# Kernel tuning notes

Hardware: AMD Instinct MI355X
Metric: run time of the kernel (lower is better)

Reference implementation:

```python
import jax, jax.numpy as jnp
import numpy as np
import math

B, T, C = 8, 1024, 512
H = 8
HD = C // H  # 64
MAX_REL = 64 + 4  # args.block_size + args.time_cond


def setup_inputs() -> dict:
    key = jax.random.key(0)
    ks = jax.random.split(key, 12)
    xavier = lambda k, shape: jax.random.uniform(
        k, shape, jnp.float32, -1.0, 1.0) * math.sqrt(6.0 / (shape[0] + shape[1]))
    return {
        "x": jax.random.normal(ks[0], (B, T, C), jnp.float32),
        "Wq": xavier(ks[1], (C, C)), "bq": jnp.zeros((C,), jnp.float32),
        "Wk": xavier(ks[2], (C, C)), "bk": jnp.zeros((C,), jnp.float32),
        "Wv": xavier(ks[3], (C, C)), "bv": jnp.zeros((C,), jnp.float32),
        "Wo": xavier(ks[4], (C, C)), "bo": jnp.zeros((C,), jnp.float32),
        "rel_k": xavier(ks[5], (2 * MAX_REL + 1, HD)),
        "rel_v": xavier(ks[6], (2 * MAX_REL + 1, HD)),
    }


def _rel_index(t):
    # clipped relative distance matrix, shifted to [0, 2*MAX_REL]
    r = jnp.arange(t)
    dist = jnp.clip(r[None, :] - r[:, None], -MAX_REL, MAX_REL)
    return dist + MAX_REL  # (T, T) int32


def reference(x, Wq, bq, Wk, bk, Wv, bv, Wo, bo, rel_k, rel_v):
    b, t, c = x.shape
    h, hd = H, HD
    q = x @ Wq + bq
    k = x @ Wk + bk
    v = x @ Wv + bv
    rq = q.reshape(b, t, h, hd).transpose(0, 2, 1, 3)  # (B,H,T,hd)
    rk = k.reshape(b, t, h, hd).transpose(0, 2, 1, 3)
    rv = v.reshape(b, t, h, hd).transpose(0, 2, 1, 3)

    idx = _rel_index(t)                 # (T,T)
    rk2 = rel_k[idx]                    # (T,T,hd)
    rv2 = rel_v[idx]                    # (T,T,hd)

    attn1 = jnp.einsum("bhqd,bhkd->bhqk", rq, rk)
    attn2 = jnp.einsum("bhqd,qkd->bhqk", rq, rk2)
    # NOTE: original scales by 1/sqrt(embed_dim) (k.size(-1) == C), not head_dim
    attn = jax.nn.softmax((attn1 + attn2) * (1.0 / math.sqrt(c)), axis=-1)

    w1 = jnp.einsum("bhqk,bhkd->bhqd", attn, rv)
    w2 = jnp.einsum("bhqk,qkd->bhqd", attn, rv2)
    out = (w1 + w2).transpose(0, 2, 1, 3).reshape(b, t, c)
    return out @ Wo + bo
```

## Files before the change

### kernel.cpp

```cpp
#include <hip/hip_runtime.h>
#include <stdint.h>

#define Bb 8
#define Tt 1024
#define Cc 512
#define Hh 8
#define HD 64
#define MREL 68
#define NR 137
#define NRP 160
#define A2S 168
#define SCALE 0.044194173824159216f
#define KSCL  0.063763016845703125f

typedef unsigned short u16;
typedef unsigned int u32;
using u16x4  = __attribute__((ext_vector_type(4))) u16;
using u16x8  = __attribute__((ext_vector_type(8))) u16;
using f32x4  = __attribute__((ext_vector_type(4))) float;
using bf16x8 = __attribute__((ext_vector_type(8))) __bf16;

__device__ __forceinline__ u16 f2bf(float f) {
  u32 u = __builtin_bit_cast(u32, f);
  u += 0x7FFF + ((u >> 16) & 1);
  return (u16)(u >> 16);
}
__device__ __forceinline__ float bf2f(u16 v) {
  return __builtin_bit_cast(float, (u32)v << 16);
}
__device__ __forceinline__ bf16x8 as_bf8(u16x8 v) { return __builtin_bit_cast(bf16x8, v); }
__device__ __forceinline__ float fexp2(float x) {
  float r; asm("v_exp_f32 %0, %1" : "=v"(r) : "v"(x)); return r;
}

#define MFMA16(a, b, c) __builtin_amdgcn_mfma_f32_16x16x32_bf16((a), (b), (c), 0, 0, 0)
#define PSWZ(row, col) ((col) ^ (((row) & 7) << 3))

__global__ __launch_bounds__(256) void relv_prep(
    const float* __restrict__ rel_v, u16* __restrict__ rvT)
{
  int i = blockIdx.x * 256 + threadIdx.x;
  if (i < HD * NRP) {
    int d = i / NRP, r = i - d * NRP;
    rvT[i] = (r < NR) ? f2bf(rel_v[r * HD + d]) : (u16)0;
  }
}

__global__ __launch_bounds__(256) void w_prep(
    const float* __restrict__ Wq, const float* __restrict__ Wk,
    const float* __restrict__ Wv, const float* __restrict__ Wo,
    u16* __restrict__ WqT, u16* __restrict__ WkT,
    u16* __restrict__ WvT, u16* __restrict__ WoT)
{
  const float* W = blockIdx.y == 0 ? Wq : blockIdx.y == 1 ? Wk
                  : blockIdx.y == 2 ? Wv : Wo;
  u16* WT = blockIdx.y == 0 ? WqT : blockIdx.y == 1 ? WkT
           : blockIdx.y == 2 ? WvT : WoT;
  int i = blockIdx.x * 256 + threadIdx.x;
  int n = i >> 7, k4 = (i & 127) * 4;
  u16x4 o;
  #pragma unroll
  for (int j = 0; j < 4; ++j) o[j] = f2bf(W[(size_t)(k4 + j) * Cc + n]);
  *(u16x4*)&WT[(size_t)n * Cc + k4] = o;
}

__global__ __launch_bounds__(256) void qkv_gemm(
    const float* __restrict__ x,
    const u16* __restrict__ WqT, const u16* __restrict__ WkT,
    const u16* __restrict__ WvT,
    const float* __restrict__ bq, const float* __restrict__ bk,
    const float* __restrict__ bv,
    u16* __restrict__ Qb, u16* __restrict__ Kb, u16* __restrict__ VTb)
{
  __shared__ u16 Xs[64][40];
  __shared__ u16 WTs[3][64][40];

  const u16* Wp[3] = {WqT, WkT, WvT};
  const float* bp[3] = {bq, bk, bv};

  const int tid = threadIdx.x;
  const int wv_ = tid >> 6;
  const int l   = tid & 63;
  const int lr  = l & 15, lg = l >> 4;
  const int m0  = blockIdx.x * 64;
  const int n0  = blockIdx.y * 64;
  const int srow = tid >> 2, scol = (tid & 3) * 8;

  f32x4 acc[3][4];
  #pragma unroll
  for (int a = 0; a < 3; ++a)
    #pragma unroll
    for (int b = 0; b < 4; ++b) acc[a][b] = (f32x4){0.f, 0.f, 0.f, 0.f};

  for (int k0 = 0; k0 < Cc; k0 += 32) {
    {
      const float* xp = x + (size_t)(m0 + srow) * Cc + k0 + scol;
      f32x4 v0 = *(const f32x4*)xp;
      f32x4 v1 = *(const f32x4*)(xp + 4);
      u16x8 o = {f2bf(v0[0]), f2bf(v0[1]), f2bf(v0[2]), f2bf(v0[3]),
                 f2bf(v1[0]), f2bf(v1[1]), f2bf(v1[2]), f2bf(v1[3])};
      *(u16x8*)&Xs[srow][scol] = o;
    }
    #pragma unroll
    for (int q3 = 0; q3 < 3; ++q3) {
      u16x8 w = *(const u16x8*)(Wp[q3] + (size_t)(n0 + srow) * Cc + k0 + scol);
      *(u16x8*)&WTs[q3][srow][scol] = w;
    }
    __syncthreads();

    bf16x8 a = as_bf8(*(const u16x8*)&Xs[wv_ * 16 + lr][lg * 8]);
    #pragma unroll
    for (int q3 = 0; q3 < 3; ++q3) {
      #pragma unroll
      for (int nt = 0; nt < 4; ++nt) {
        bf16x8 b = as_bf8(*(const u16x8*)&WTs[q3][nt * 16 + lr][lg * 8]);
        acc[q3][nt] = MFMA16(a, b, acc[q3][nt]);
      }
    }
    __syncthreads();
  }

  const int bidx = m0 >> 10;
  #pragma unroll
  for (int q3 = 0; q3 < 3; ++q3) {
    #pragma unroll
    for (int nt = 0; nt < 4; ++nt) {
      int n = n0 + nt * 16 + lr;
      int h = n >> 6, d = n & 63;
      float bias = bp[q3][n];
      #pragma unroll
      for (int i = 0; i < 4; ++i) {
        int m = m0 + wv_ * 16 + lg * 4 + i;
        int t = m & (Tt - 1);
        u16 o = f2bf(acc[q3][nt][i] + bias);
        size_t bh = (size_t)(bidx * Hh + h);
        if (q3 == 0)      Qb[(bh * Tt + t) * HD + d] = o;
        else if (q3 == 1) Kb[(bh * Tt + t) * HD + d] = o;
        else              VTb[(bh * HD + d) * Tt + t] = o;
      }
    }
  }
}

__global__ __launch_bounds__(256, 4) void attn_kernel(
    const u16* __restrict__ Qb, const u16* __restrict__ Kb,
    const u16* __restrict__ VTb, const u16* __restrict__ rvT,
    const float* __restrict__ rel_k,
    u16* __restrict__ AO)
{
  __shared__ u16 P[16][1024];
  __shared__ u16 S2a2[16][A2S];
  __shared__ float red[2][4][16];
  __shared__ float rowrcp[16];

  const int tid = threadIdx.x;
  const int wv_ = tid >> 6, l = tid & 63;
  const int lr = l & 15, lg = l >> 4;
  const int bh = blockIdx.x;
  const int q0 = blockIdx.y * 16;
  const int bidx = bh >> 3, h = bh & 7;

  const u16* Qh = Qb  + (size_t)bh * Tt * HD;
  const u16* Kh = Kb  + (size_t)bh * Tt * HD;
  const u16* Vh = VTb + (size_t)bh * HD * Tt;

  bf16x8 aQ0 = as_bf8(*(const u16x8*)(Qh + (size_t)(q0 + lr) * HD + lg * 8));
  bf16x8 aQ1 = as_bf8(*(const u16x8*)(Qh + (size_t)(q0 + lr) * HD + 32 + lg * 8));

  const u16* kbase = Kh + (size_t)(wv_ * 16 + lr) * HD + lg * 8;
  u16x8 c0 = *(const u16x8*)(kbase);
  u16x8 c1 = *(const u16x8*)(kbase + 32);

  for (int ct = wv_; ct < 9; ct += 4) {
    int r = ct * 16 + lr;
    f32x4 acc = {0.f, 0.f, 0.f, 0.f};
    #pragma unroll
    for (int d0 = 0; d0 < 64; d0 += 32) {
      u16x8 bbits = {0, 0, 0, 0, 0, 0, 0, 0};
      if (r < NR) {
        f32x4 v0 = *(const f32x4*)(rel_k + (size_t)r * HD + d0 + lg * 8);
        f32x4 v1 = *(const f32x4*)(rel_k + (size_t)r * HD + d0 + lg * 8 + 4);
        bbits = (u16x8){f2bf(v0[0]), f2bf(v0[1]), f2bf(v0[2]), f2bf(v0[3]),
                        f2bf(v1[0]), f2bf(v1[1]), f2bf(v1[2]), f2bf(v1[3])};
      }
      acc = MFMA16(d0 ? aQ1 : aQ0, as_bf8(bbits), acc);
    }
    #pragma unroll
    for (int i = 0; i < 4; ++i)
      S2a2[lg * 4 + i][ct * 16 + lr] = f2bf(acc[i] * KSCL);
  }
  __syncthreads();

  float ps[4]  = {0.f, 0.f, 0.f, 0.f};
  float ps0[4] = {0.f, 0.f, 0.f, 0.f};

  #pragma unroll
  for (int kt = 0; kt < 16; ++kt) {
    u16x8 n0{}, n1{};
    if (kt < 15) {
      n0 = *(const u16x8*)(kbase + (size_t)(kt + 1) * 64 * HD);
      n1 = *(const u16x8*)(kbase + (size_t)(kt + 1) * 64 * HD + 32);
    }
    int kc = kt * 64 + wv_ * 16 + lr;
    f32x4 acc = {0.f, 0.f, 0.f, 0.f};
    acc = MFMA16(aQ0, as_bf8(c0), acc);
    acc = MFMA16(aQ1, as_bf8(c1), acc);
    int b2 = kc - q0 - lg * 4;
    #pragma unroll
    for (int i = 0; i < 4; ++i) {
      int row = lg * 4 + i;
      int dr = b2 - i;
      dr = dr < -MREL ? -MREL : (dr > MREL ? MREL : dr);
      float p = fexp2(fmaf(acc[i], KSCL, bf2f(S2a2[row][dr + MREL])));
      ps[i] += p;
      if (kc <= q0 + row - MREL) ps0[i] += p;
      P[row][PSWZ(row, kc)] = f2bf(p);
    }
    if (kt < 15) { c0 = n0; c1 = n1; }
  }

  #pragma unroll
  for (int off = 1; off < 16; off <<= 1) {
    #pragma unroll
    for (int i = 0; i < 4; ++i) {
      ps[i]  += __shfl_xor(ps[i], off);
      ps0[i] += __shfl_xor(ps0[i], off);
    }
  }
  if (lr == 0) {
    #pragma unroll
    for (int i = 0; i < 4; ++i) {
      red[0][wv_][lg * 4 + i] = ps[i];
      red[1][wv_][lg * 4 + i] = ps0[i];
    }
  }

  const u16* vrow = Vh + (size_t)(wv_ * 16 + lr) * Tt + lg * 8;
  u16x8 vc0 = *(const u16x8*)(vrow);
  u16x8 vc1 = *(const u16x8*)(vrow + 32);

  __syncthreads();

  {
    int row = tid >> 4, c16 = tid & 15;
    int qg = q0 + row;
    float band = 0.f;
    for (int r = 1 + c16; r < NR - 1; r += 16) {
      int k = qg + r - MREL;
      u16 v = (k >= 0 && k < Tt) ? P[row][PSWZ(row, k)] : (u16)0;
      S2a2[row][r] = v;
      band += bf2f(v);
    }
    #pragma unroll
    for (int off = 1; off < 16; off <<= 1) band += __shfl_xor(band, off);
    for (int r = NR + c16; r < NRP; r += 16) S2a2[row][r] = 0;
    if (c16 == 0) {
      float t0 = red[0][0][row] + red[0][1][row] + red[0][2][row] + red[0][3][row];
      float t1 = red[1][0][row] + red[1][1][row] + red[1][2][row] + red[1][3][row];
      S2a2[row][0]      = f2bf(t1);
      S2a2[row][NR - 1] = f2bf(t0 - t1 - band);
      rowrcp[row] = 1.0f / t0;
    }
  }
  __syncthreads();

  f32x4 o0 = {0.f, 0.f, 0.f, 0.f}, o1 = {0.f, 0.f, 0.f, 0.f};
  #pragma unroll
  for (int kp = 0; kp < 15; ++kp) {
    u16x8 vn0 = *(const u16x8*)(vrow + kp * 64 + 64);
    u16x8 vn1 = *(const u16x8*)(vrow + kp * 64 + 96);
    bf16x8 a0 = as_bf8(*(const u16x8*)&P[lr][PSWZ(lr, kp * 64 + lg * 8)]);
    bf16x8 a1 = as_bf8(*(const u16x8*)&P[lr][PSWZ(lr, kp * 64 + 32 + lg * 8)]);
    o0 = MFMA16(a0, as_bf8(vc0), o0);
    o1 = MFMA16(a1, as_bf8(vc1), o1);
    vc0 = vn0; vc1 = vn1;
  }
  {
    bf16x8 a0 = as_bf8(*(const u16x8*)&P[lr][PSWZ(lr, 15 * 64 + lg * 8)]);
    bf16x8 a1 = as_bf8(*(const u16x8*)&P[lr][PSWZ(lr, 15 * 64 + 32 + lg * 8)]);
    o0 = MFMA16(a0, as_bf8(vc0), o0);
    o1 = MFMA16(a1, as_bf8(vc1), o1);
  }
  #pragma unroll
  for (int j = 0; j < 5; ++j) {
    u16x8 brv = *(const u16x8*)(rvT + (size_t)(wv_ * 16 + lr) * NRP + j * 32 + lg * 8);
    bf16x8 aa = as_bf8(*(const u16x8*)&S2a2[lr][j * 32 + lg * 8]);
    if (j & 1) o1 = MFMA16(aa, as_bf8(brv), o1);
    else       o0 = MFMA16(aa, as_bf8(brv), o0);
  }

  #pragma unroll
  for (int i = 0; i < 4; ++i) {
    int row = lg * 4 + i;
    float val = (o0[i] + o1[i]) * rowrcp[row];
    int t = q0 + row, cc = h * HD + wv_ * 16 + lr;
    AO[((size_t)(bidx * Tt + t)) * Cc + cc] = f2bf(val);
  }
}

__global__ __launch_bounds__(256) void out_gemm(
    const u16* __restrict__ AO, const u16* __restrict__ WoT,
    const float* __restrict__ bo, float* __restrict__ out)
{
  __shared__ u16 As[64][40];
  __shared__ u16 WTs[64][40];
  const int tid = threadIdx.x;
  const int wv_ = tid >> 6, l = tid & 63, lr = l & 15, lg = l >> 4;
  const int m0 = blockIdx.x * 64, n0 = blockIdx.y * 64;
  const int srow = tid >> 2, scol = (tid & 3) * 8;

  f32x4 acc[4];
  #pragma unroll
  for (int b = 0; b < 4; ++b) acc[b] = (f32x4){0.f, 0.f, 0.f, 0.f};

  for (int k0 = 0; k0 < Cc; k0 += 32) {
    u16x8 av = *(const u16x8*)(AO + (size_t)(m0 + srow) * Cc + k0 + scol);
    *(u16x8*)&As[srow][scol] = av;
    u16x8 wv2 = *(const u16x8*)(WoT + (size_t)(n0 + srow) * Cc + k0 + scol);
    *(u16x8*)&WTs[srow][scol] = wv2;
    __syncthreads();

    bf16x8 a = as_bf8(*(const u16x8*)&As[wv_ * 16 + lr][lg * 8]);
    #pragma unroll
    for (int nt = 0; nt < 4; ++nt) {
      bf16x8 b = as_bf8(*(const u16x8*)&WTs[nt * 16 + lr][lg * 8]);
      acc[nt] = MFMA16(a, b, acc[nt]);
    }
    __syncthreads();
  }

  #pragma unroll
  for (int nt = 0; nt < 4; ++nt) {
    int n = n0 + nt * 16 + lr;
    float bias = bo[n];
    #pragma unroll
    for (int i = 0; i < 4; ++i) {
      int m = m0 + wv_ * 16 + lg * 4 + i;
      out[(size_t)m * Cc + n] = acc[nt][i] + bias;
    }
  }
}

extern "C" void kernel_launch(void* const* d_in, const int* in_sizes, int n_in,
                              void* d_out, int out_size, void* d_ws, size_t ws_size,
                              hipStream_t stream) {
  const float* x  = (const float*)d_in[0];
  const float* Wq = (const float*)d_in[1];
  const float* bq = (const float*)d_in[2];
  const float* Wk = (const float*)d_in[3];
  const float* bk = (const float*)d_in[4];
  const float* Wv = (const float*)d_in[5];
  const float* bv = (const float*)d_in[6];
  const float* Wo = (const float*)d_in[7];
  const float* bo = (const float*)d_in[8];
  const float* rk = (const float*)d_in[9];
  const float* rv = (const float*)d_in[10];

  const size_t BHTD = (size_t)Bb * Hh * Tt * HD;
  const size_t WSZ  = (size_t)Cc * Cc;

  u16* Qb = (u16*)d_out;
  u16* Kb = Qb + BHTD;
  u16* VT  = (u16*)d_ws;
  u16* AO  = VT + BHTD;
  u16* rvT = AO + BHTD;
  u16* WqT = rvT + (size_t)HD * NRP;
  u16* WkT = WqT + WSZ;
  u16* WvT = WkT + WSZ;
  u16* WoT = WvT + WSZ;
  float* outf = (float*)d_out;

  relv_prep<<<dim3((HD * NRP + 255) / 256), 256, 0, stream>>>(rv, rvT);
  w_prep<<<dim3(256, 4), 256, 0, stream>>>(Wq, Wk, Wv, Wo, WqT, WkT, WvT, WoT);
  qkv_gemm<<<dim3(128, 8), 256, 0, stream>>>(x, WqT, WkT, WvT, bq, bk, bv, Qb, Kb, VT);
  attn_kernel<<<dim3(64, 64), 256, 0, stream>>>(Qb, Kb, VT, rvT, rk, AO);
  out_gemm<<<dim3(128, 8), 256, 0, stream>>>(AO, WoT, bo, outf);
}
```

Measured before the change: 209.6 us.

## Transpose score MFMA, skip band lookups outside clipped region, pack bf16 stores

Swaps the MFMA operands so each lane holds four consecutive keys for a single query row. Outside the relative-position band the bias is a constant, so those key tiles skip the per-element LDS bias lookup and the band-mask check. P values are packed two at a time with v_cvt_pk_bf16_f32 and written as 64-bit stores. The row-sum reduction shrinks from four shuffle steps over four values to two steps over one value. This adds branchy per-tile logic whose range bounds must be right.

```diff
diff --git a/kernel.cpp b/kernel.cpp
--- a/kernel.cpp
+++ b/kernel.cpp
@@ -17,6 +17,7 @@
 typedef unsigned int u32;
 using u16x4  = __attribute__((ext_vector_type(4))) u16;
 using u16x8  = __attribute__((ext_vector_type(8))) u16;
+using u32x2  = __attribute__((ext_vector_type(2))) u32;
 using f32x4  = __attribute__((ext_vector_type(4))) float;
 using bf16x8 = __attribute__((ext_vector_type(8))) __bf16;
 
@@ -31,6 +32,9 @@
 __device__ __forceinline__ bf16x8 as_bf8(u16x8 v) { return __builtin_bit_cast(bf16x8, v); }
 __device__ __forceinline__ float fexp2(float x) {
   float r; asm("v_exp_f32 %0, %1" : "=v"(r) : "v"(x)); return r;
+}
+__device__ __forceinline__ u32 cvtpk(float lo, float hi) {
+  u32 r; asm("v_cvt_pk_bf16_f32 %0, %1, %2" : "=v"(r) : "v"(lo), "v"(hi)); return r;
 }
 
 #define MFMA16(a, b, c) __builtin_amdgcn_mfma_f32_16x16x32_bf16((a), (b), (c), 0, 0, 0)
@@ -191,8 +195,15 @@
   }
   __syncthreads();
 
-  float ps[4]  = {0.f, 0.f, 0.f, 0.f};
-  float ps0[4] = {0.f, 0.f, 0.f, 0.f};
+  const int qme = q0 + lr;
+  const float cN = bf2f(S2a2[lr][0]);
+  const float cP = bf2f(S2a2[lr][NR - 1]);
+
+  int lowEnd  = (q0 >= 131) ? (((q0 - 131) >> 6) + 1) : 0;
+  int hiStart = (q0 + 146) >> 6; if (hiStart > 16) hiStart = 16;
+
+  float ps = 0.f, ps0 = 0.f;
+  const int kcb = wv_ * 16 + lg * 4;
 
   #pragma unroll
   for (int kt = 0; kt < 16; ++kt) {
@@ -201,39 +212,36 @@
       n0 = *(const u16x8*)(kbase + (size_t)(kt + 1) * 64 * HD);
       n1 = *(const u16x8*)(kbase + (size_t)(kt + 1) * 64 * HD + 32);
     }
-    int kc = kt * 64 + wv_ * 16 + lr;
     f32x4 acc = {0.f, 0.f, 0.f, 0.f};
-    acc = MFMA16(aQ0, as_bf8(c0), acc);
-    acc = MFMA16(aQ1, as_bf8(c1), acc);
-    int b2 = kc - q0 - lg * 4;
-    #pragma unroll
-    for (int i = 0; i < 4; ++i) {
-      int row = lg * 4 + i;
-      int dr = b2 - i;
-      dr = dr < -MREL ? -MREL : (dr > MREL ? MREL : dr);
-      float p = fexp2(fmaf(acc[i], KSCL, bf2f(S2a2[row][dr + MREL])));
-      ps[i] += p;
-      if (kc <= q0 + row - MREL) ps0[i] += p;
-      P[row][PSWZ(row, kc)] = f2bf(p);
-    }
+    acc = MFMA16(as_bf8(c0), aQ0, acc);
+    acc = MFMA16(as_bf8(c1), aQ1, acc);
+    int kc = kt * 64 + kcb;
+    float p[4];
+    if (kt >= lowEnd && kt < hiStart) {
+      #pragma unroll
+      for (int i = 0; i < 4; ++i) {
+        int dr = kc + i - qme;
+        dr = dr < -MREL ? -MREL : (dr > MREL ? MREL : dr);
+        p[i] = fexp2(fmaf(acc[i], KSCL, bf2f(S2a2[lr][dr + MREL])));
+        if (kc + i <= qme - MREL) ps0 += p[i];
+      }
+      ps += (p[0] + p[1]) + (p[2] + p[3]);
+    } else {
+      float c = (kt < lowEnd) ? cN : cP;
+      #pragma unroll
+      for (int i = 0; i < 4; ++i) p[i] = fexp2(fmaf(acc[i], KSCL, c));
+      float s4 = (p[0] + p[1]) + (p[2] + p[3]);
+      ps += s4;
+      if (kt < lowEnd) ps0 += s4;
+    }
+    u32x2 pw = {cvtpk(p[0], p[1]), cvtpk(p[2], p[3])};
+    *(u32x2*)&P[lr][PSWZ(lr, kc)] = pw;
     if (kt < 15) { c0 = n0; c1 = n1; }
   }
 
-  #pragma unroll
-  for (int off = 1; off < 16; off <<= 1) {
-    #pragma unroll
-    for (int i = 0; i < 4; ++i) {
-      ps[i]  += __shfl_xor(ps[i], off);
-      ps0[i] += __shfl_xor(ps0[i], off);
-    }
-  }
-  if (lr == 0) {
-    #pragma unroll
-    for (int i = 0; i < 4; ++i) {
-      red[0][wv_][lg * 4 + i] = ps[i];
-      red[1][wv_][lg * 4 + i] = ps0[i];
-    }
-  }
+  ps  += __shfl_xor(ps, 16);  ps  += __shfl_xor(ps, 32);
+  ps0 += __shfl_xor(ps0, 16); ps0 += __shfl_xor(ps0, 32);
+  if (lg == 0) { red[0][wv_][lr] = ps; red[1][wv_][lr] = ps0; }
 
   const u16* vrow = Vh + (size_t)(wv_ * 16 + lr) * Tt + lg * 8;
   u16x8 vc0 = *(const u16x8*)(vrow);
```

Result: no change. 209.1 us (-0.2%).
